# Kernel optimization log

Measured on AMD Instinct MI355X. Metric: run time of the kernel, lower is better.

The kernel has to match this reference:

```python
import jax, jax.numpy as jnp
import numpy as np

EMB = 1024
HID = 4096
NHEADS = 16
DK = EMB // NHEADS
EPS = 1e-6
B, S = 2, 2048


def setup_inputs() -> dict:
    key = jax.random.key(0)
    ks = jax.random.split(key, 10)
    sc = 0.02
    return {
        "x": jax.random.normal(ks[0], (B, S, EMB), dtype=jnp.float32),
        "src_mask": jnp.ones((B, 1, 1, S), dtype=jnp.int32),
        "wq": jax.random.normal(ks[1], (EMB, EMB), dtype=jnp.float32) * sc,
        "wk": jax.random.normal(ks[2], (EMB, EMB), dtype=jnp.float32) * sc,
        "wv": jax.random.normal(ks[3], (EMB, EMB), dtype=jnp.float32) * sc,
        "wo": jax.random.normal(ks[4], (EMB, EMB), dtype=jnp.float32) * sc,
        "ff1_w": jax.random.normal(ks[5], (EMB, HID), dtype=jnp.float32) * sc,
        "ff1_b": jnp.zeros((HID,), dtype=jnp.float32),
        "ff2_w": jax.random.normal(ks[6], (HID, EMB), dtype=jnp.float32) * sc,
        "ff2_b": jnp.zeros((EMB,), dtype=jnp.float32),
        "ln1_a": jnp.ones((1,), dtype=jnp.float32),
        "ln1_b": jnp.zeros((1,), dtype=jnp.float32),
        "ln2_a": jnp.ones((1,), dtype=jnp.float32),
        "ln2_b": jnp.zeros((1,), dtype=jnp.float32),
    }


def layernorm(x, alpha, bias):
    # Faithful to the custom LayerNorm: scalar alpha/bias, std with Bessel
    # correction (torch default unbiased=True), divide by (std + eps).
    mean = jnp.mean(x, axis=-1, keepdims=True)
    var = jnp.sum((x - mean) ** 2, axis=-1, keepdims=True) / (x.shape[-1] - 1)
    std = jnp.sqrt(var)
    return alpha * (x - mean) / (std + EPS) + bias


def mha(x, mask, wq, wk, wv, wo):
    b, s, _ = x.shape
    def split_heads(t):  # [B,S,E] -> [B,H,S,dk]
        return t.reshape(b, s, NHEADS, DK).transpose(0, 2, 1, 3)
    q = split_heads(x @ wq)
    k = split_heads(x @ wk)
    v = split_heads(x @ wv)
    scores = jnp.einsum("bhqd,bhkd->bhqk", q, k) / jnp.sqrt(jnp.float32(DK))
    scores = jnp.where(mask == 0, -jnp.inf, scores)
    attn = jax.nn.softmax(scores, axis=-1)
    out = jnp.einsum("bhqk,bhkd->bhqd", attn, v)
    out = out.transpose(0, 2, 1, 3).reshape(b, s, EMB)
    return out @ wo


def ffn(x, w1, b1, w2, b2):
    return jax.nn.relu(x @ w1 + b1) @ w2 + b2


def reference(x, src_mask, wq, wk, wv, wo, ff1_w, ff1_b, ff2_w, ff2_b,
              ln1_a, ln1_b, ln2_a, ln2_b):
    # pre-norm residual encoder block (dropout=0 / eval mode)
    h = x + mha(layernorm(x, ln1_a, ln1_b), src_mask, wq, wk, wv, wo)
    out = h + ffn(layernorm(h, ln2_a, ln2_b), ff1_w, ff1_b, ff2_w, ff2_b)
    return out
```

## Files before the change

kernel.cpp:

```cpp
#include <hip/hip_runtime.h>
#include <stdint.h>

#define EMB 1024
#define HID 4096
#define NHEADS 16
#define DKH 64
#define SEQ 2048
#define BATCH 2
#define MROWS (BATCH * SEQ)
#define GBK 64

typedef unsigned short u16;
typedef unsigned int u32;
typedef __attribute__((ext_vector_type(8))) short short8;
typedef __attribute__((ext_vector_type(4))) float f32x4;
typedef __attribute__((ext_vector_type(16))) float f32x16;
typedef __attribute__((ext_vector_type(4))) u32 u32x4;
typedef __attribute__((ext_vector_type(2))) int i32x2;

#if __has_builtin(__builtin_amdgcn_exp2f)
#define QK_SCALE 0.18033688011f
#define QK_CLAMP 43.3f
__device__ __forceinline__ float pexp(float x) { return __builtin_amdgcn_exp2f(x); }
#else
#define QK_SCALE 0.125f
#define QK_CLAMP 30.0f
__device__ __forceinline__ float pexp(float x) { return __expf(x); }
#endif

__device__ __forceinline__ u16 f2bf(float f) {
    unsigned u = __float_as_uint(f);
    unsigned r = 0x7FFFu + ((u >> 16) & 1u);
    return (u16)((u + r) >> 16);
}
__device__ __forceinline__ f32x4 mfma16(short8 a, short8 b, f32x4 c) {
    return __builtin_amdgcn_mfma_f32_16x16x32_bf16(a, b, c, 0, 0, 0);
}
__device__ __forceinline__ f32x16 mfma32(short8 a, short8 b, f32x16 c) {
    return __builtin_amdgcn_mfma_f32_32x32x16_bf16(a, b, c, 0, 0, 0);
}
__device__ __forceinline__ void gl_lds16(const u16* g, u16* l) {
    __builtin_amdgcn_global_load_lds(
        (__attribute__((address_space(1))) void*)g,
        (__attribute__((address_space(3))) void*)l, 16, 0, 0);
}
__device__ __forceinline__ void plswap(u32& a, u32& b) {
#if __has_builtin(__builtin_amdgcn_permlane32_swap)
    i32x2 r = __builtin_amdgcn_permlane32_swap((int)a, (int)b, false, false);
    a = (u32)r.x; b = (u32)r.y;
#else
    const u32 ta = (u32)__shfl_xor((int)a, 32);
    const u32 tb = (u32)__shfl_xor((int)b, 32);
    const bool hi = (threadIdx.x & 32) != 0;
    const u32 na = hi ? tb : a;
    const u32 nb = hi ? b : ta;
    a = na; b = nb;
#endif
}
__device__ __forceinline__ short8 mk8(u32 a, u32 b, u32 c, u32 d) {
    u32x4 t; t.x = a; t.y = b; t.z = c; t.w = d;
    return __builtin_bit_cast(short8, t);
}

__global__ __launch_bounds__(256) void transpose_qkvo(
    const float* __restrict__ wq, const float* __restrict__ wk,
    const float* __restrict__ wv, const float* __restrict__ wo,
    u16* __restrict__ qkvT, u16* __restrict__ woT,
    const int* __restrict__ msk, int* __restrict__ flag) {
    __shared__ u16 t[32][33];
    const int z = blockIdx.z;
    const float* W = (z == 0) ? wq : (z == 1) ? wk : (z == 2) ? wv : wo;
    u16* WT = (z < 3) ? (qkvT + (size_t)z * EMB * EMB) : woT;
    const float scale = (z == 0) ? QK_SCALE : 1.0f;
    const int tx = threadIdx.x & 31, ty = threadIdx.x >> 5;
    const int k0 = blockIdx.y * 32, n0 = blockIdx.x * 32;
#pragma unroll
    for (int r = 0; r < 32; r += 8)
        t[ty + r][tx] = f2bf(scale * W[(size_t)(k0 + ty + r) * EMB + n0 + tx]);
    __syncthreads();
#pragma unroll
    for (int r = 0; r < 32; r += 8)
        WT[(size_t)(n0 + ty + r) * EMB + k0 + tx] = t[tx][ty + r];

    if (z == 3 && blockIdx.x == 0 && blockIdx.y == 0) {
        int v = 1;
        for (int i = threadIdx.x; i < BATCH * SEQ; i += 256)
            v &= (msk[i] != 0) ? 1 : 0;
        v = __all(v) ? 1 : 0;
        __shared__ int rr[4];
        if ((threadIdx.x & 63) == 0) rr[threadIdx.x >> 6] = v;
        __syncthreads();
        if (threadIdx.x == 0) flag[0] = rr[0] & rr[1] & rr[2] & rr[3];
    }
}

__global__ __launch_bounds__(256) void transpose_bf16(
    const float* __restrict__ W, u16* __restrict__ WT, int K, int N) {
    __shared__ u16 t[32][33];
    const int tx = threadIdx.x & 31, ty = threadIdx.x >> 5;
    const int k0 = blockIdx.y * 32, n0 = blockIdx.x * 32;
#pragma unroll
    for (int r = 0; r < 32; r += 8)
        t[ty + r][tx] = f2bf(W[(size_t)(k0 + ty + r) * N + n0 + tx]);
    __syncthreads();
#pragma unroll
    for (int r = 0; r < 32; r += 8)
        WT[(size_t)(n0 + ty + r) * K + k0 + tx] = t[tx][ty + r];
}

__global__ __launch_bounds__(256) void ln_kernel(
    const float* __restrict__ x, u16* __restrict__ out,
    const float* __restrict__ alpha_p, const float* __restrict__ beta_p) {
    const int row = blockIdx.x;
    const int tid = threadIdx.x;
    float4 v = reinterpret_cast<const float4*>(x + (size_t)row * EMB)[tid];

    __shared__ float red[4];
    float s = v.x + v.y + v.z + v.w;
    for (int off = 32; off; off >>= 1) s += __shfl_down(s, off);
    if ((tid & 63) == 0) red[tid >> 6] = s;
    __syncthreads();
    float mean = (red[0] + red[1] + red[2] + red[3]) * (1.0f / EMB);
    __syncthreads();

    float d0 = v.x - mean, d1 = v.y - mean, d2 = v.z - mean, d3 = v.w - mean;
    float sq = d0 * d0 + d1 * d1 + d2 * d2 + d3 * d3;
    for (int off = 32; off; off >>= 1) sq += __shfl_down(sq, off);
    if ((tid & 63) == 0) red[tid >> 6] = sq;
    __syncthreads();
    float var = (red[0] + red[1] + red[2] + red[3]) * (1.0f / (EMB - 1));
    float inv = 1.0f / (sqrtf(var) + 1e-6f);
    float a = alpha_p[0], b = beta_p[0];

    ushort4 o;
    o.x = f2bf(a * d0 * inv + b);
    o.y = f2bf(a * d1 * inv + b);
    o.z = f2bf(a * d2 * inv + b);
    o.w = f2bf(a * d3 * inv + b);
    reinterpret_cast<ushort4*>(out + (size_t)row * EMB)[tid] = o;
}

template <int BN, int NWM>
__global__ __launch_bounds__(512) void gemm_mfma(
    const u16* __restrict__ A, const u16* __restrict__ BT, void* C,
    const float* __restrict__ bias, const void* res,
    int M, int N, int K, int relu, int out_mode,
    u16* __restrict__ Kb_out, u16* __restrict__ VT_out) {
    constexpr int NWN = 8 / NWM;
    constexpr int WM = 128 / (16 * NWM);
    constexpr int WN = BN / (16 * NWN);
    constexpr int NBUF = (BN == 64) ? 3 : 2;
    __shared__ u16 As[NBUF][128][GBK];
    __shared__ u16 Bs[NBUF][BN][GBK];

    const int tid = threadIdx.x;
    const int wave = tid >> 6, lane = tid & 63;
    const int quad = lane >> 4, lc = lane & 15;
    const int wm = wave % NWM, wn = wave / NWM;

    const int nx = gridDim.x;
    const int bid = blockIdx.y * nx + blockIdx.x;
    const int xcd = bid & 7, sl = bid >> 3;
    const int nyx = gridDim.y >> 3;
    const int bcol = sl % nx;
    const int brow = (sl / nx) + xcd * nyx;
    const int row0 = brow * 128, col0 = bcol * BN;

    const int srow = lane >> 3;
    const int scg = (lane & 7) ^ srow;

    f32x4 acc[WM][WN] = {};

    auto stage = [&](int k0, int buf) {
#pragma unroll
        for (int i = 0; i < 2; ++i) {
            const int rb = wave * 16 + i * 8;
            gl_lds16(A + (size_t)(row0 + rb + srow) * K + k0 + scg * 8,
                     &As[buf][rb][0]);
        }
        if constexpr (BN == 128) {
#pragma unroll
            for (int i = 0; i < 2; ++i) {
                const int rb = wave * 16 + i * 8;
                gl_lds16(BT + (size_t)(col0 + rb + srow) * K + k0 + scg * 8,
                         &Bs[buf][rb][0]);
            }
        } else {
            const int rb = wave * 8;
            gl_lds16(BT + (size_t)(col0 + rb + srow) * K + k0 + scg * 8,
                     &Bs[buf][rb][0]);
        }
    };

    auto compute = [&](int cur) {
#pragma unroll
        for (int s = 0; s < 2; ++s) {
            short8 af[WM], bfv[WN];
#pragma unroll
            for (int i = 0; i < WM; ++i) {
                const int ar = wm * (16 * WM) + i * 16 + lc;
                af[i] = *reinterpret_cast<const short8*>(
                    &As[cur][ar][(((s * 4 + quad) ^ (ar & 7))) * 8]);
            }
#pragma unroll
            for (int j = 0; j < WN; ++j) {
                const int br = wn * (16 * WN) + j * 16 + lc;
                bfv[j] = *reinterpret_cast<const short8*>(
                    &Bs[cur][br][(((s * 4 + quad) ^ (br & 7))) * 8]);
            }
#pragma unroll
            for (int i = 0; i < WM; ++i)
#pragma unroll
                for (int j = 0; j < WN; ++j)
                    acc[i][j] = mfma16(af[i], bfv[j], acc[i][j]);
        }
    };

    if constexpr (NBUF == 2) {
        stage(0, 0);
        __syncthreads();
        int cur = 0;
        for (int k0 = 0; k0 < K; k0 += GBK) {
            if (k0 + GBK < K) stage(k0 + GBK, cur ^ 1);
            compute(cur);
            __syncthreads();
            cur ^= 1;
        }
    } else {
        stage(0, 0);
        if (GBK < K) stage(GBK, 1);
        int cur = 0;
        for (int k0 = 0; k0 < K; k0 += GBK) {
            if (k0 + 2 * GBK < K) {
                int nb = cur + 2; if (nb >= 3) nb -= 3;
                stage(k0 + 2 * GBK, nb);
            }
            const int rem = (K - k0) >> 6;
            if (rem > 2)       asm volatile("s_waitcnt vmcnt(6)" ::: "memory");
            else if (rem == 2) asm volatile("s_waitcnt vmcnt(3)" ::: "memory");
            else               asm volatile("s_waitcnt vmcnt(0)" ::: "memory");
            __builtin_amdgcn_s_barrier();
            __builtin_amdgcn_sched_barrier(0);
            compute(cur);
            __builtin_amdgcn_s_barrier();
            cur = (cur == 2) ? 0 : cur + 1;
        }
    }

    u16* Cb = (u16*)C;
    int mode = out_mode, ncols = N, lcol0 = col0;
    if (out_mode == 3) {
        const int seg = col0 >> 10;
        lcol0 = col0 & 1023;
        ncols = EMB;
        if (seg == 1) { Cb = Kb_out; mode = 0; }
        else if (seg == 2) { Cb = VT_out; mode = 2; }
        else { mode = 0; }
    }

#pragma unroll
    for (int j = 0; j < WN; ++j) {
        const int col = lcol0 + wn * (16 * WN) + j * 16 + lc;
        const float bv = bias ? bias[col] : 0.f;
#pragma unroll
        for (int i = 0; i < WM; ++i) {
            const int rbase = row0 + wm * (16 * WM) + i * 16 + quad * 4;
            if (mode == 2) {
                ushort4 o;
                o.x = f2bf(acc[i][j][0]); o.y = f2bf(acc[i][j][1]);
                o.z = f2bf(acc[i][j][2]); o.w = f2bf(acc[i][j][3]);
                *reinterpret_cast<ushort4*>(Cb + (size_t)col * M + rbase) = o;
            } else {
#pragma unroll
                for (int r = 0; r < 4; ++r) {
                    const size_t idx = (size_t)(rbase + r) * ncols + col;
                    float v = acc[i][j][r] + bv;
                    if (relu) v = fmaxf(v, 0.f);
                    if (res) v += ((const float*)res)[idx];
                    if (mode == 1) ((float*)C)[idx] = v;
                    else Cb[idx] = f2bf(v);
                }
            }
        }
    }
}

__global__ __launch_bounds__(512, 4) void attn_mfma(
    const u16* __restrict__ Q, const u16* __restrict__ K,
    const u16* __restrict__ VT, const int* __restrict__ mask,
    const int* __restrict__ mflag, u16* __restrict__ O) {
    const int tid = threadIdx.x;
    const int wave = tid >> 6, lane = tid & 63;
    const int hi = lane >> 5, ln31 = lane & 31;
    const int qt = wave >> 1, s = wave & 1;
    const int H = blockIdx.x & 31;
    const int qblk = blockIdx.x >> 5;
    const int h = H & 15, b = H >> 4;

    __shared__ __align__(16) char smem[65536];
    u16 (*Ks)[128][DKH] = (u16(*)[128][DKH])smem;
    u16 (*Vs)[DKH][128] = (u16(*)[DKH][128])(smem + 32768);

    const int fast = mflag[0];

    const u16* qp = Q + (size_t)(b * SEQ + qblk * 128 + qt * 32 + ln31) * EMB
                      + h * DKH + hi * 8;
    short8 qb[4];
#pragma unroll
    for (int f = 0; f < 4; ++f)
        qb[f] = *reinterpret_cast<const short8*>(qp + f * 16);

    const int srow = lane >> 3, scg = (lane & 7) ^ srow;
    const int svr = lane >> 4, ssl = lane & 15;

    auto stage = [&](int kc, int buf) {
#pragma unroll
        for (int i = 0; i < 2; ++i) {
            const int t8 = wave * 16 + i * 8;
            gl_lds16(K + (size_t)(b * SEQ + kc + t8 + srow) * EMB + h * DKH + scg * 8,
                     &Ks[buf][t8][0]);
        }
#pragma unroll
        for (int i = 0; i < 2; ++i) {
            const int d4 = wave * 8 + i * 4;
            const int dim = d4 + svr;
            const int gv = ssl ^ (dim & 15);
            gl_lds16(VT + (size_t)(h * DKH + dim) * MROWS + b * SEQ + kc + gv * 8,
                     &Vs[buf][d4][0]);
        }
    };

    f32x16 o0 = {}, o1 = {};
    float rs = 0.f;
    const int tok0 = s * 64;

    stage(0, 0);
    __syncthreads();
    int cur = 0;

    for (int kc = 0; kc < SEQ; kc += 128) {
        if (kc + 128 < SEQ) stage(kc + 128, cur ^ 1);

#pragma unroll
        for (int mt = 0; mt < 2; ++mt) {
            const int trow = tok0 + mt * 32 + ln31;
            f32x16 st = {};
#pragma unroll
            for (int f = 0; f < 4; ++f) {
                const int slot = (2 * f + hi) ^ (trow & 7);
                const short8 ka = *reinterpret_cast<const short8*>(
                    &Ks[cur][trow][slot * 8]);
                st = mfma32(ka, qb[f], st);
            }
            if (fast) {
#pragma unroll
                for (int r = 0; r < 16; ++r)
                    st[r] = pexp(fminf(st[r], QK_CLAMP));
            } else {
#pragma unroll
                for (int g = 0; g < 4; ++g) {
                    const int4 mk = *reinterpret_cast<const int4*>(
                        mask + b * SEQ + kc + tok0 + mt * 32 + g * 8 + hi * 4);
                    const int* mkp = &mk.x;
#pragma unroll
                    for (int r4 = 0; r4 < 4; ++r4) {
                        const int r = g * 4 + r4;
                        const float pv = pexp(fminf(st[r], QK_CLAMP));
                        st[r] = mkp[r4] ? pv : 0.f;
                    }
                }
            }
            rs += (((st[0] + st[1]) + (st[2] + st[3])) +
                   ((st[4] + st[5]) + (st[6] + st[7]))) +
                  (((st[8] + st[9]) + (st[10] + st[11])) +
                   ((st[12] + st[13]) + (st[14] + st[15])));

            u32 pk0 = __builtin_amdgcn_perm(__float_as_uint(st[1]),
                                            __float_as_uint(st[0]), 0x07060302u);
            u32 pk1 = __builtin_amdgcn_perm(__float_as_uint(st[3]),
                                            __float_as_uint(st[2]), 0x07060302u);
            u32 pk2 = __builtin_amdgcn_perm(__float_as_uint(st[5]),
                                            __float_as_uint(st[4]), 0x07060302u);
            u32 pk3 = __builtin_amdgcn_perm(__float_as_uint(st[7]),
                                            __float_as_uint(st[6]), 0x07060302u);
            u32 pk4 = __builtin_amdgcn_perm(__float_as_uint(st[9]),
                                            __float_as_uint(st[8]), 0x07060302u);
            u32 pk5 = __builtin_amdgcn_perm(__float_as_uint(st[11]),
                                            __float_as_uint(st[10]), 0x07060302u);
            u32 pk6 = __builtin_amdgcn_perm(__float_as_uint(st[13]),
                                            __float_as_uint(st[12]), 0x07060302u);
            u32 pk7 = __builtin_amdgcn_perm(__float_as_uint(st[15]),
                                            __float_as_uint(st[14]), 0x07060302u);
            plswap(pk0, pk2);
            plswap(pk1, pk3);
            plswap(pk4, pk6);
            plswap(pk5, pk7);
            const short8 fr0 = mk8(pk0, pk1, pk2, pk3);
            const short8 fr1 = mk8(pk4, pk5, pk6, pk7);

#pragma unroll
            for (int sub = 0; sub < 2; ++sub) {
                const short8 fr = sub ? fr1 : fr0;
                const int g = s * 8 + (2 * mt + sub) * 2 + hi;
#pragma unroll
                for (int nt = 0; nt < 2; ++nt) {
                    const int drow = nt * 32 + ln31;
                    const short8 vb = *reinterpret_cast<const short8*>(
                        &Vs[cur][drow][(g ^ (drow & 15)) * 8]);
                    if (nt == 0) o0 = mfma32(fr, vb, o0);
                    else         o1 = mfma32(fr, vb, o1);
                }
            }
        }
        __syncthreads();
        cur ^= 1;
    }

    rs += __shfl_xor(rs, 32);

    float* Om = (float*)smem;
    float* Ls = (float*)(smem + 34816);

    if (s == 0) {
#pragma unroll
        for (int nt = 0; nt < 2; ++nt)
#pragma unroll
            for (int r = 0; r < 16; ++r) {
                const int row = (r & 3) + 8 * (r >> 2) + 4 * hi;
                Om[(qt * 32 + row) * 68 + nt * 32 + ln31] = nt ? o1[r] : o0[r];
            }
        if (lane < 32) Ls[qt * 32 + ln31] = rs;
    }
    __syncthreads();
    if (s == 1) {
        const float lt = rs + Ls[qt * 32 + ln31];
        if (lane < 32) Ls[qt * 32 + ln31] = lt;
#pragma unroll
        for (int nt = 0; nt < 2; ++nt)
#pragma unroll
            for (int r = 0; r < 16; ++r) {
                const int row = (r & 3) + 8 * (r >> 2) + 4 * hi;
                const int idx = (qt * 32 + row) * 68 + nt * 32 + ln31;
                Om[idx] += nt ? o1[r] : o0[r];
            }
    }
    __syncthreads();

    {
        const int q = tid >> 2, seg = tid & 3;
        const float inv = 1.0f / Ls[q];
        const float* src = Om + q * 68 + seg * 16;
        u16* dst = O + (size_t)(b * SEQ + qblk * 128 + q) * EMB + h * DKH + seg * 16;
#pragma unroll
        for (int i = 0; i < 4; ++i) {
            const float4 v = *reinterpret_cast<const float4*>(src + i * 4);
            ushort4 ou;
            ou.x = f2bf(v.x * inv); ou.y = f2bf(v.y * inv);
            ou.z = f2bf(v.z * inv); ou.w = f2bf(v.w * inv);
            *reinterpret_cast<ushort4*>(dst + i * 4) = ou;
        }
    }
}

extern "C" void kernel_launch(void* const* d_in, const int* in_sizes, int n_in,
                              void* d_out, int out_size, void* d_ws, size_t ws_size,
                              hipStream_t stream) {
    const float* x     = (const float*)d_in[0];
    const int*   mask  = (const int*)d_in[1];
    const float* wq    = (const float*)d_in[2];
    const float* wk    = (const float*)d_in[3];
    const float* wv    = (const float*)d_in[4];
    const float* wo    = (const float*)d_in[5];
    const float* ff1_w = (const float*)d_in[6];
    const float* ff1_b = (const float*)d_in[7];
    const float* ff2_w = (const float*)d_in[8];
    const float* ff2_b = (const float*)d_in[9];
    const float* ln1_a = (const float*)d_in[10];
    const float* ln1_b = (const float*)d_in[11];
    const float* ln2_a = (const float*)d_in[12];
    const float* ln2_b = (const float*)d_in[13];
    float* out = (float*)d_out;

    char* ws = (char*)d_ws;
    const size_t MB = 1u << 20;
    u16* act   = (u16*)(ws + 0);
    u16* Qb    = (u16*)(ws + 8 * MB);
    u16* Kb    = (u16*)(ws + 16 * MB);
    u16* VTb   = (u16*)(ws + 24 * MB);
    int* mflag = (int*)(ws + 32 * MB);
    u16* f1    = (u16*)(ws + 8 * MB);
    u16* wqkvT = (u16*)(ws + 40 * MB);
    u16* woT   = (u16*)(ws + 46 * MB);
    u16* ffT   = (u16*)(ws + 40 * MB);

    transpose_qkvo<<<dim3(EMB / 32, EMB / 32, 4), 256, 0, stream>>>(
        wq, wk, wv, wo, wqkvT, woT, mask, mflag);

    ln_kernel<<<MROWS, 256, 0, stream>>>(x, act, ln1_a, ln1_b);

    gemm_mfma<128, 2><<<dim3(3 * EMB / 128, MROWS / 128), 512, 0, stream>>>(
        act, wqkvT, Qb, nullptr, nullptr, MROWS, 3 * EMB, EMB, 0, 3, Kb, VTb);

    attn_mfma<<<BATCH * NHEADS * (SEQ / 128), 512, 0, stream>>>(
        Qb, Kb, VTb, mask, mflag, act);

    gemm_mfma<64, 4><<<dim3(EMB / 64, MROWS / 128), 512, 0, stream>>>(
        act, woT, out, nullptr, x, MROWS, EMB, EMB, 0, 1, nullptr, nullptr);

    ln_kernel<<<MROWS, 256, 0, stream>>>(out, act, ln2_a, ln2_b);

    transpose_bf16<<<dim3(HID / 32, EMB / 32), 256, 0, stream>>>(ff1_w, ffT, EMB, HID);
    gemm_mfma<128, 2><<<dim3(HID / 128, MROWS / 128), 512, 0, stream>>>(
        act, ffT, f1, ff1_b, nullptr, MROWS, HID, EMB, 1, 0, nullptr, nullptr);

    transpose_bf16<<<dim3(EMB / 32, HID / 32), 256, 0, stream>>>(ff2_w, ffT, HID, EMB);
    gemm_mfma<64, 4><<<dim3(EMB / 64, MROWS / 128), 512, 0, stream>>>(
        f1, ffT, out, ff2_b, out, MROWS, EMB, HID, 0, 1, nullptr, nullptr);
}
```

Before: 345.8 us.

## Add 256-thread GEMM with 64x64 per-wave tiles for FFN layers

```diff
diff --git a/kernel.cpp b/kernel.cpp
--- a/kernel.cpp
+++ b/kernel.cpp
@@ -283,6 +283,101 @@
             }
         }
     }
+}
+
+__global__ __launch_bounds__(256) void gemm_w64(
+    const u16* __restrict__ A, const u16* __restrict__ BT, void* C,
+    const float* __restrict__ bias, const void* res,
+    int M, int N, int K, int relu, int fp32out) {
+    __shared__ u16 As[2][128][GBK];
+    __shared__ u16 Bs[2][128][GBK];
+
+    const int tid = threadIdx.x;
+    const int wave = tid >> 6, lane = tid & 63;
+    const int hi = lane >> 5, ln31 = lane & 31;
+    const int wm = wave >> 1, wn = wave & 1;
+
+    const int nx = gridDim.x;
+    const int bid = blockIdx.y * nx + blockIdx.x;
+    const int xcd = bid & 7, sl = bid >> 3;
+    const int nyx = gridDim.y >> 3;
+    const int bcol = sl % nx;
+    const int brow = (sl / nx) + xcd * nyx;
+    const int row0 = brow * 128, col0 = bcol * 128;
+
+    const int srow = lane >> 3;
+    const int scg = (lane & 7) ^ srow;
+
+    f32x16 a00 = {}, a01 = {}, a10 = {}, a11 = {};
+
+    auto stage = [&](int k0, int buf) {
+#pragma unroll
+        for (int i = 0; i < 4; ++i) {
+            const int rb = wave * 32 + i * 8;
+            gl_lds16(A + (size_t)(row0 + rb + srow) * K + k0 + scg * 8,
+                     &As[buf][rb][0]);
+        }
+#pragma unroll
+        for (int i = 0; i < 4; ++i) {
+            const int rb = wave * 32 + i * 8;
+            gl_lds16(BT + (size_t)(col0 + rb + srow) * K + k0 + scg * 8,
+                     &Bs[buf][rb][0]);
+        }
+    };
+
+    const int nt = K >> 6;
+    stage(0, 0);
+    int cur = 0;
+    for (int t = 0; t < nt; ++t) {
+        if (t + 1 < nt) {
+            stage((t + 1) << 6, cur ^ 1);
+            asm volatile("s_waitcnt vmcnt(8)" ::: "memory");
+        } else {
+            asm volatile("s_waitcnt vmcnt(0)" ::: "memory");
+        }
+        __builtin_amdgcn_s_barrier();
+        __builtin_amdgcn_sched_barrier(0);
+
+#pragma unroll
+        for (int s = 0; s < 4; ++s) {
+            const int slb = ((2 * s + hi) ^ (ln31 & 7)) * 8;
+            const short8 fa0 = *reinterpret_cast<const short8*>(
+                &As[cur][wm * 64 + ln31][slb]);
+            const short8 fa1 = *reinterpret_cast<const short8*>(
+                &As[cur][wm * 64 + 32 + ln31][slb]);
+            const short8 fb0 = *reinterpret_cast<const short8*>(
+                &Bs[cur][wn * 64 + ln31][slb]);
+            const short8 fb1 = *reinterpret_cast<const short8*>(
+                &Bs[cur][wn * 64 + 32 + ln31][slb]);
+            a00 = mfma32(fa0, fb0, a00);
+            a01 = mfma32(fa0, fb1, a01);
+            a10 = mfma32(fa1, fb0, a10);
+            a11 = mfma32(fa1, fb1, a11);
+        }
+        __builtin_amdgcn_s_barrier();
+        cur ^= 1;
+    }
+
+#pragma unroll
+    for (int ti = 0; ti < 2; ++ti)
+#pragma unroll
+        for (int tj = 0; tj < 2; ++tj) {
+            const f32x16& av = (ti == 0) ? (tj == 0 ? a00 : a01)
+                                         : (tj == 0 ? a10 : a11);
+            const int col = col0 + wn * 64 + tj * 32 + ln31;
+            const float bv = bias ? bias[col] : 0.f;
+            const int rb2 = row0 + wm * 64 + ti * 32 + 4 * hi;
+#pragma unroll
+            for (int r = 0; r < 16; ++r) {
+                const int row = rb2 + (r & 3) + 8 * (r >> 2);
+                const size_t idx = (size_t)row * N + col;
+                float v = av[r] + bv;
+                if (relu) v = fmaxf(v, 0.f);
+                if (res) v += ((const float*)res)[idx];
+                if (fp32out) ((float*)C)[idx] = v;
+                else ((u16*)C)[idx] = f2bf(v);
+            }
+        }
 }
 
 __global__ __launch_bounds__(512, 4) void attn_mfma(
@@ -510,10 +605,10 @@
     ln_kernel<<<MROWS, 256, 0, stream>>>(out, act, ln2_a, ln2_b);
 
     transpose_bf16<<<dim3(HID / 32, EMB / 32), 256, 0, stream>>>(ff1_w, ffT, EMB, HID);
-    gemm_mfma<128, 2><<<dim3(HID / 128, MROWS / 128), 512, 0, stream>>>(
-        act, ffT, f1, ff1_b, nullptr, MROWS, HID, EMB, 1, 0, nullptr, nullptr);
+    gemm_w64<<<dim3(HID / 128, MROWS / 128), 256, 0, stream>>>(
+        act, ffT, f1, ff1_b, nullptr, MROWS, HID, EMB, 1, 0);
 
     transpose_bf16<<<dim3(EMB / 32, HID / 32), 256, 0, stream>>>(ff2_w, ffT, HID, EMB);
-    gemm_mfma<64, 4><<<dim3(EMB / 64, MROWS / 128), 512, 0, stream>>>(
-        f1, ffT, out, ff2_b, out, MROWS, EMB, HID, 0, 1, nullptr, nullptr);
-}
+    gemm_w64<<<dim3(EMB / 128, MROWS / 128), 256, 0, stream>>>(
+        f1, ffT, out, ff2_b, out, MROWS, EMB, HID, 0, 1);
+}
```

Result: slower. 380.3 us (+10.0%).
